# Optimization experiments

Measured on AMD Instinct MI355X. Metric: run time of the kernel, lower is better.

The kernel has to match this reference:

```python
import jax, jax.numpy as jnp
import numpy as np

N_MOD, DEPTH, DIM_E = 8, 2, 128   # n experts, routing depth, codebook dim
C, H, W, B = 128, 32, 32, 16      # channels, spatial, batch


def setup_inputs() -> dict:
    key = jax.random.key(0)
    ks = jax.random.split(key, 5)
    s = lambda fan: 1.0 / np.sqrt(fan)
    x = jax.random.normal(ks[0], (B, C, H, W), jnp.float32)
    # controller: 1x1 conv == linear on globally-pooled features
    W_ctl = jax.random.normal(ks[1], (DEPTH * DIM_E, C), jnp.float32) * s(C)
    b_ctl = jnp.zeros((DEPTH * DIM_E,), jnp.float32)
    # VQ codebook: [dim_embeddings, n_modules]
    emb = jax.random.normal(ks[2], (DIM_E, N_MOD), jnp.float32)
    # expert conv weights (shared across depth, as in the module list)
    W_exp = jax.random.normal(ks[3], (N_MOD, C, C, 3, 3), jnp.float32) * s(C * 9)
    b_exp = jnp.zeros((N_MOD, C), jnp.float32)
    return {"x": x, "W_ctl": W_ctl, "b_ctl": b_ctl, "emb": emb,
            "W_exp": W_exp, "b_exp": b_exp}


def reference(x, W_ctl, b_ctl, emb, W_exp, b_exp):
    Bn = x.shape[0]
    # controller: 1x1 conv then AdaptiveAvgPool2d(1) == pool then linear
    pooled = x.mean(axis=(2, 3))                      # [B, C]
    ctl = (pooled @ W_ctl.T + b_ctl).reshape(Bn, DIM_E, DEPTH)  # [B, D, depth]
    # nearest-embedding routing indices (argmin over codebook, no grad path)
    d2 = ((ctl[:, :, :, None] - emb[None, :, None, :]) ** 2).sum(axis=1)  # [B, depth, n_mod]
    idx = jnp.argmin(d2, axis=-1)                     # [B, depth]
    # quantized controller codes from detached ctl (same indices here)
    ctl_sg = jax.lax.stop_gradient(ctl)
    d2n = ((ctl_sg[:, :, :, None] - emb[None, :, None, :]) ** 2).sum(axis=1)
    idx_n = jnp.argmin(d2n, axis=-1)                  # [B, depth]
    ctl_nearest = jnp.transpose(emb[:, idx_n], (1, 0, 2))  # [B, D, depth]
    # dispatch: run all experts as one grouped conv, then gather per example
    Wflat = W_exp.reshape(N_MOD * C, C, 3, 3)
    y = x
    for t in range(DEPTH):
        out = jax.lax.conv_general_dilated(
            y, Wflat, window_strides=(1, 1), padding='SAME',
            dimension_numbers=('NCHW', 'OIHW', 'NCHW'))  # [B, n_mod*C, H, W]
        out = out.reshape(Bn, N_MOD, C, H, W) + b_exp[None, :, :, None, None]
        out = jax.nn.relu(out)
        y = out[jnp.arange(Bn), idx[:, t]]            # [B, C, H, W]
    return y, ctl, ctl_nearest
```

## Files before the change

### kernel.cpp

```cpp
#include <hip/hip_runtime.h>
#include <cstddef>

#define NMOD   8
#define DEPTH_ 2
#define DIME   128
#define CCH    128
#define HH     32
#define WW     32
#define BB     16
#define HWPX   (HH*WW)

#define CO_TILE 4
#define CI_TILE 4
#define TROWS   34
#define TSTRIDE 36
#define PF_N    4

__global__ __launch_bounds__(256) void pool_kernel(
    const float* __restrict__ x, float* __restrict__ pooled)
{
    const int ch   = blockIdx.x * 4 + (threadIdx.x >> 6);
    const int lane = threadIdx.x & 63;
    const float* xc = x + (size_t)ch * HWPX;

    float4 s4 = {0.f, 0.f, 0.f, 0.f};
    #pragma unroll
    for (int k = 0; k < 4; ++k) {
        const float4 v = *(const float4*)(xc + (size_t)(lane + k * 64) * 4);
        s4.x += v.x; s4.y += v.y; s4.z += v.z; s4.w += v.w;
    }
    float s = (s4.x + s4.y) + (s4.z + s4.w);
    #pragma unroll
    for (int off = 32; off; off >>= 1) s += __shfl_xor(s, off, 64);
    if (lane == 0) pooled[ch] = s * (1.0f / HWPX);
}

__global__ __launch_bounds__(256) void ctl_kernel(
    const float* __restrict__ pooled, const float* __restrict__ W_ctl,
    const float* __restrict__ b_ctl, const float* __restrict__ emb,
    float* __restrict__ ctl_out, float* __restrict__ ctln_out,
    int* __restrict__ idx_out)
{
    const int b   = blockIdx.x;
    const int tid = threadIdx.x;

    __shared__ float pld[CCH];
    __shared__ float ctlrow[DIME * DEPTH_];
    __shared__ float d2s[DEPTH_ * NMOD];
    __shared__ int   sidx[DEPTH_];

    if (tid < CCH / 4)
        ((float4*)pld)[tid] = ((const float4*)(pooled + (size_t)b * CCH))[tid];
    __syncthreads();

    {
        const float4* wr = (const float4*)(W_ctl + (size_t)tid * CCH);
        const float4* pv = (const float4*)pld;
        float a0 = 0.f, a1 = 0.f, a2 = 0.f, a3 = 0.f;
        #pragma unroll
        for (int k = 0; k < 32; k += 4) {
            const float4 w0 = wr[k + 0], p0 = pv[k + 0];
            const float4 w1 = wr[k + 1], p1 = pv[k + 1];
            const float4 w2 = wr[k + 2], p2 = pv[k + 2];
            const float4 w3 = wr[k + 3], p3 = pv[k + 3];
            a0 = fmaf(w0.x, p0.x, fmaf(w0.y, p0.y, fmaf(w0.z, p0.z, fmaf(w0.w, p0.w, a0))));
            a1 = fmaf(w1.x, p1.x, fmaf(w1.y, p1.y, fmaf(w1.z, p1.z, fmaf(w1.w, p1.w, a1))));
            a2 = fmaf(w2.x, p2.x, fmaf(w2.y, p2.y, fmaf(w2.z, p2.z, fmaf(w2.w, p2.w, a2))));
            a3 = fmaf(w3.x, p3.x, fmaf(w3.y, p3.y, fmaf(w3.z, p3.z, fmaf(w3.w, p3.w, a3))));
        }
        const float s = b_ctl[tid] + ((a0 + a1) + (a2 + a3));
        ctlrow[tid] = s;
        ctl_out[(size_t)b * (DIME * DEPTH_) + tid] = s;
    }
    __syncthreads();

    {
        const int p = tid >> 4;
        const int sub = tid & 15;
        const int t = p >> 3, mm = p & 7;
        float s = 0.f;
        #pragma unroll
        for (int k = 0; k < 8; ++k) {
            const int e = sub * 8 + k;
            const float d = ctlrow[e * DEPTH_ + t] - emb[e * NMOD + mm];
            s = fmaf(d, d, s);
        }
        #pragma unroll
        for (int off = 8; off; off >>= 1) s += __shfl_xor(s, off, 16);
        if (sub == 0) d2s[p] = s;
    }
    __syncthreads();

    if (tid < DEPTH_) {
        float best = d2s[tid * NMOD];
        int bi = 0;
        for (int m = 1; m < NMOD; ++m) {
            const float d = d2s[tid * NMOD + m];
            if (d < best) { best = d; bi = m; }
        }
        sidx[tid] = bi;
        idx_out[b * DEPTH_ + tid] = bi;
    }
    __syncthreads();

    {
        const int e = tid >> 1, t = tid & 1;
        ctln_out[(size_t)b * (DIME * DEPTH_) + e * DEPTH_ + t] =
            emb[e * NMOD + sidx[t]];
    }
}

__global__ __launch_bounds__(256, 2) void conv_kernel(
    const float* __restrict__ in, const float* __restrict__ W_exp,
    const float* __restrict__ b_exp, const int* __restrict__ idx,
    int t, float* __restrict__ out)
{
    const int cog = blockIdx.x;
    const int b   = blockIdx.y;
    const int tid = threadIdx.x;
    const int m   = __builtin_amdgcn_readfirstlane(idx[b * DEPTH_ + t]);
    const int co0 = cog * CO_TILE;

    __shared__ float wlds[CCH * 9 * CO_TILE];
    __shared__ float tile[CI_TILE * TROWS * TSTRIDE];

    const float* wg = W_exp + ((size_t)m * CCH + co0) * (CCH * 9);
    for (int i = tid; i < CO_TILE * CCH * 9; i += 256) {
        int co = i / (CCH * 9);
        int r  = i - co * (CCH * 9);
        wlds[r * CO_TILE + co] = wg[(size_t)co * (CCH * 9) + r];
    }
    for (int i = tid; i < CI_TILE * TROWS * TSTRIDE; i += 256) tile[i] = 0.f;

    const int h  = tid >> 3;
    const int w4 = (tid & 7) * 4;

    float acc[4][CO_TILE];
    #pragma unroll
    for (int p = 0; p < 4; ++p)
        #pragma unroll
        for (int c = 0; c < CO_TILE; ++c) acc[p][c] = 0.f;

    const float* inb = in + (size_t)b * CCH * HWPX;

    float4 pf[PF_N];
    #pragma unroll
    for (int k = 0; k < PF_N; ++k)
        pf[k] = *(const float4*)(inb + (size_t)(tid + k * 256) * 4);

    __syncthreads();

    for (int ci0 = 0; ci0 < CCH; ci0 += CI_TILE) {
        #pragma unroll
        for (int k = 0; k < PF_N; ++k) {
            const int q   = tid + k * 256;
            const int cil = q >> 8;
            const int p4  = q & 255;
            const int hh  = p4 >> 3;
            const int ww  = (p4 & 7) * 4;
            float* dst = &tile[cil * (TROWS * TSTRIDE) + (hh + 1) * TSTRIDE + (ww + 1)];
            dst[0] = pf[k].x; dst[1] = pf[k].y; dst[2] = pf[k].z; dst[3] = pf[k].w;
        }
        if (ci0 + CI_TILE < CCH) {
            const float* src = inb + (size_t)(ci0 + CI_TILE) * HWPX;
            #pragma unroll
            for (int k = 0; k < PF_N; ++k)
                pf[k] = *(const float4*)(src + (size_t)(tid + k * 256) * 4);
        }
        __syncthreads();

        #pragma unroll
        for (int cil = 0; cil < CI_TILE; ++cil) {
            const float* trow = &tile[cil * (TROWS * TSTRIDE)];
            const float* wrow = &wlds[(size_t)(ci0 + cil) * 9 * CO_TILE];
            #pragma unroll
            for (int kh = 0; kh < 3; ++kh) {
                const float* r = trow + (h + kh) * TSTRIDE + w4;
                const float4 a4 = *(const float4*)(r);
                const float2 a2 = *(const float2*)(r + 4);
                const float in6[6] = {a4.x, a4.y, a4.z, a4.w, a2.x, a2.y};
                #pragma unroll
                for (int kw = 0; kw < 3; ++kw) {
                    const float4 wa = *(const float4*)(wrow + (kh * 3 + kw) * CO_TILE);
                    #pragma unroll
                    for (int p = 0; p < 4; ++p) {
                        const float v = in6[p + kw];
                        acc[p][0] = fmaf(v, wa.x, acc[p][0]);
                        acc[p][1] = fmaf(v, wa.y, acc[p][1]);
                        acc[p][2] = fmaf(v, wa.z, acc[p][2]);
                        acc[p][3] = fmaf(v, wa.w, acc[p][3]);
                    }
                }
            }
        }
        __syncthreads();
    }

    const float* be = b_exp + (size_t)m * CCH + co0;
    float* ob = out + ((size_t)b * CCH + co0) * HWPX + h * WW + w4;
    #pragma unroll
    for (int c = 0; c < CO_TILE; ++c) {
        const float bv = be[c];
        float4 v;
        v.x = fmaxf(acc[0][c] + bv, 0.f);
        v.y = fmaxf(acc[1][c] + bv, 0.f);
        v.z = fmaxf(acc[2][c] + bv, 0.f);
        v.w = fmaxf(acc[3][c] + bv, 0.f);
        *(float4*)(ob + (size_t)c * HWPX) = v;
    }
}

extern "C" void kernel_launch(void* const* d_in, const int* in_sizes, int n_in,
                              void* d_out, int out_size, void* d_ws, size_t ws_size,
                              hipStream_t stream) {
    const float* x     = (const float*)d_in[0];
    const float* W_ctl = (const float*)d_in[1];
    const float* b_ctl = (const float*)d_in[2];
    const float* emb   = (const float*)d_in[3];
    const float* W_exp = (const float*)d_in[4];
    const float* b_exp = (const float*)d_in[5];

    float* out      = (float*)d_out;
    float* y_out    = out;
    float* ctl_out  = out + (size_t)BB * CCH * HWPX;
    float* ctln_out = ctl_out + BB * DIME * DEPTH_;

    float* y1     = (float*)d_ws;
    int*   idxp   = (int*)((char*)d_ws + (size_t)BB * CCH * HWPX * sizeof(float));
    float* pooled = (float*)((char*)idxp + 128);

    pool_kernel<<<(BB * CCH) / 4, 256, 0, stream>>>(x, pooled);
    ctl_kernel<<<BB, 256, 0, stream>>>(pooled, W_ctl, b_ctl, emb,
                                       ctl_out, ctln_out, idxp);
    conv_kernel<<<dim3(CCH / CO_TILE, BB), 256, 0, stream>>>(
        x, W_exp, b_exp, idxp, 0, y1);
    conv_kernel<<<dim3(CCH / CO_TILE, BB), 256, 0, stream>>>(
        y1, W_exp, b_exp, idxp, 1, y_out);
}
```

Baseline: 240.4 us.

## Split conv input channels across two thread groups with LDS reduction

The conv kernel now launches 512 threads per block. Two 256-thread groups each handle half of the input channels in their own LDS tile, and group 1's partial sums are reduced into group 0 through shared memory before the bias and ReLU epilogue. The tile layout also moves to aligned float4 stores, with left and right halo loads taken as scalar reads. This doubles the number of waves per block to hide latency, at the cost of extra LDS, a reduction pass, and a tighter register budget from launch_bounds(512,4).

New measurement: 320.3 us. 33.2% more time.

```diff
diff --git a/kernel.cpp b/kernel.cpp
--- a/kernel.cpp
+++ b/kernel.cpp
@@ -15,6 +15,8 @@
 #define TROWS   34
 #define TSTRIDE 36
 #define PF_N    4
+#define SLAB_F  (TROWS * TSTRIDE)
+#define TILE_G  (CI_TILE * SLAB_F + 4)
 
 __global__ __launch_bounds__(256) void pool_kernel(
     const float* __restrict__ x, float* __restrict__ pooled)
@@ -110,30 +112,33 @@
     }
 }
 
-__global__ __launch_bounds__(256, 2) void conv_kernel(
+__global__ __launch_bounds__(512, 4) void conv_kernel(
     const float* __restrict__ in, const float* __restrict__ W_exp,
     const float* __restrict__ b_exp, const int* __restrict__ idx,
     int t, float* __restrict__ out)
 {
-    const int cog = blockIdx.x;
-    const int b   = blockIdx.y;
-    const int tid = threadIdx.x;
+    const int cog  = blockIdx.x;
+    const int b    = blockIdx.y;
+    const int tid  = threadIdx.x;
+    const int g    = tid >> 8;
+    const int tid2 = tid & 255;
     const int m   = __builtin_amdgcn_readfirstlane(idx[b * DEPTH_ + t]);
     const int co0 = cog * CO_TILE;
 
     __shared__ float wlds[CCH * 9 * CO_TILE];
-    __shared__ float tile[CI_TILE * TROWS * TSTRIDE];
+    __shared__ __align__(16) float tile[2 * TILE_G];
+    float* mytile = tile + g * TILE_G + 4;
 
     const float* wg = W_exp + ((size_t)m * CCH + co0) * (CCH * 9);
-    for (int i = tid; i < CO_TILE * CCH * 9; i += 256) {
+    for (int i = tid; i < CO_TILE * CCH * 9; i += 512) {
         int co = i / (CCH * 9);
         int r  = i - co * (CCH * 9);
         wlds[r * CO_TILE + co] = wg[(size_t)co * (CCH * 9) + r];
     }
-    for (int i = tid; i < CI_TILE * TROWS * TSTRIDE; i += 256) tile[i] = 0.f;
-
-    const int h  = tid >> 3;
-    const int w4 = (tid & 7) * 4;
+    for (int i = tid; i < 2 * TILE_G; i += 512) tile[i] = 0.f;
+
+    const int h  = tid2 >> 3;
+    const int w4 = (tid2 & 7) * 4;
 
     float acc[4][CO_TILE];
     #pragma unroll
@@ -141,44 +146,45 @@
         #pragma unroll
         for (int c = 0; c < CO_TILE; ++c) acc[p][c] = 0.f;
 
-    const float* inb = in + (size_t)b * CCH * HWPX;
+    const float* inb  = in + (size_t)b * CCH * HWPX;
+    const float* ing  = inb + (size_t)g * 64 * HWPX;
 
     float4 pf[PF_N];
     #pragma unroll
     for (int k = 0; k < PF_N; ++k)
-        pf[k] = *(const float4*)(inb + (size_t)(tid + k * 256) * 4);
-
-    __syncthreads();
-
-    for (int ci0 = 0; ci0 < CCH; ci0 += CI_TILE) {
+        pf[k] = *(const float4*)(ing + (size_t)(tid2 + k * 256) * 4);
+
+    __syncthreads();
+
+    for (int ci0 = 0; ci0 < 64; ci0 += CI_TILE) {
         #pragma unroll
         for (int k = 0; k < PF_N; ++k) {
-            const int q   = tid + k * 256;
+            const int q   = tid2 + k * 256;
             const int cil = q >> 8;
             const int p4  = q & 255;
             const int hh  = p4 >> 3;
             const int ww  = (p4 & 7) * 4;
-            float* dst = &tile[cil * (TROWS * TSTRIDE) + (hh + 1) * TSTRIDE + (ww + 1)];
-            dst[0] = pf[k].x; dst[1] = pf[k].y; dst[2] = pf[k].z; dst[3] = pf[k].w;
-        }
-        if (ci0 + CI_TILE < CCH) {
-            const float* src = inb + (size_t)(ci0 + CI_TILE) * HWPX;
+            *(float4*)(mytile + cil * SLAB_F + (hh + 1) * TSTRIDE + ww) = pf[k];
+        }
+        if (ci0 + CI_TILE < 64) {
+            const float* src = ing + (size_t)(ci0 + CI_TILE) * HWPX;
             #pragma unroll
             for (int k = 0; k < PF_N; ++k)
-                pf[k] = *(const float4*)(src + (size_t)(tid + k * 256) * 4);
+                pf[k] = *(const float4*)(src + (size_t)(tid2 + k * 256) * 4);
         }
         __syncthreads();
 
         #pragma unroll
         for (int cil = 0; cil < CI_TILE; ++cil) {
-            const float* trow = &tile[cil * (TROWS * TSTRIDE)];
-            const float* wrow = &wlds[(size_t)(ci0 + cil) * 9 * CO_TILE];
+            const float* slab = mytile + cil * SLAB_F;
+            const float* wrow = &wlds[(size_t)(g * 64 + ci0 + cil) * 9 * CO_TILE];
             #pragma unroll
             for (int kh = 0; kh < 3; ++kh) {
-                const float* r = trow + (h + kh) * TSTRIDE + w4;
-                const float4 a4 = *(const float4*)(r);
-                const float2 a2 = *(const float2*)(r + 4);
-                const float in6[6] = {a4.x, a4.y, a4.z, a4.w, a2.x, a2.y};
+                const float* r = slab + (h + kh) * TSTRIDE + w4;
+                const float  l0 = r[-1];
+                const float4 a4 = *(const float4*)r;
+                const float  r5 = r[4];
+                const float in6[6] = {l0, a4.x, a4.y, a4.z, a4.w, r5};
                 #pragma unroll
                 for (int kw = 0; kw < 3; ++kw) {
                     const float4 wa = *(const float4*)(wrow + (kh * 3 + kw) * CO_TILE);
@@ -196,17 +202,28 @@
         __syncthreads();
     }
 
-    const float* be = b_exp + (size_t)m * CCH + co0;
-    float* ob = out + ((size_t)b * CCH + co0) * HWPX + h * WW + w4;
-    #pragma unroll
-    for (int c = 0; c < CO_TILE; ++c) {
-        const float bv = be[c];
-        float4 v;
-        v.x = fmaxf(acc[0][c] + bv, 0.f);
-        v.y = fmaxf(acc[1][c] + bv, 0.f);
-        v.z = fmaxf(acc[2][c] + bv, 0.f);
-        v.w = fmaxf(acc[3][c] + bv, 0.f);
-        *(float4*)(ob + (size_t)c * HWPX) = v;
+    float* scratch = tile + TILE_G;
+    if (g == 1) {
+        #pragma unroll
+        for (int p = 0; p < 4; ++p)
+            #pragma unroll
+            for (int c = 0; c < CO_TILE; ++c)
+                scratch[(p * CO_TILE + c) * 256 + tid2] = acc[p][c];
+    }
+    __syncthreads();
+    if (g == 0) {
+        const float* be = b_exp + (size_t)m * CCH + co0;
+        float* ob = out + ((size_t)b * CCH + co0) * HWPX + h * WW + w4;
+        #pragma unroll
+        for (int c = 0; c < CO_TILE; ++c) {
+            const float bv = be[c];
+            float4 v;
+            v.x = fmaxf(acc[0][c] + scratch[(0 * CO_TILE + c) * 256 + tid2] + bv, 0.f);
+            v.y = fmaxf(acc[1][c] + scratch[(1 * CO_TILE + c) * 256 + tid2] + bv, 0.f);
+            v.z = fmaxf(acc[2][c] + scratch[(2 * CO_TILE + c) * 256 + tid2] + bv, 0.f);
+            v.w = fmaxf(acc[3][c] + scratch[(3 * CO_TILE + c) * 256 + tid2] + bv, 0.f);
+            *(float4*)(ob + (size_t)c * HWPX) = v;
+        }
     }
 }
 
@@ -232,8 +249,8 @@
     pool_kernel<<<(BB * CCH) / 4, 256, 0, stream>>>(x, pooled);
     ctl_kernel<<<BB, 256, 0, stream>>>(pooled, W_ctl, b_ctl, emb,
                                        ctl_out, ctln_out, idxp);
-    conv_kernel<<<dim3(CCH / CO_TILE, BB), 256, 0, stream>>>(
+    conv_kernel<<<dim3(CCH / CO_TILE, BB), 512, 0, stream>>>(
         x, W_exp, b_exp, idxp, 0, y1);
-    conv_kernel<<<dim3(CCH / CO_TILE, BB), 256, 0, stream>>>(
+    conv_kernel<<<dim3(CCH / CO_TILE, BB), 512, 0, stream>>>(
         y1, W_exp, b_exp, idxp, 1, y_out);
 }
```
